# Kernel tuning notes

Measured on AMD Instinct MI355X. Metric: run time of the kernel, lower is better.

## Reference

```python
import jax, jax.numpy as jnp
import numpy as np

N_HEADS = 16
N_KV_HEADS = 4
HEAD_DIM = 128  # n_embd // n_head = 2048 // 16
NEG_INF = -1e9


def setup_inputs() -> dict:
    key = jax.random.key(0)
    ks = jax.random.split(key, 4)
    B, T, C = 8, 1024, 2048
    x = jax.random.normal(ks[0], (B, T, C), dtype=jnp.float32)
    sc = 1.0 / np.sqrt(C)
    Wq = jax.random.normal(ks[1], (C, C), dtype=jnp.float32) * sc
    bq = jnp.zeros((C,), dtype=jnp.float32)
    Wkv = jax.random.normal(ks[2], (N_KV_HEADS * HEAD_DIM * 2, C), dtype=jnp.float32) * sc
    bkv = jnp.zeros((N_KV_HEADS * HEAD_DIM * 2,), dtype=jnp.float32)
    Wo = jax.random.normal(ks[3], (C, C), dtype=jnp.float32) * sc
    bo = jnp.zeros((C,), dtype=jnp.float32)
    return {"x": x, "Wq": Wq, "bq": bq, "Wkv": Wkv, "bkv": bkv, "Wo": Wo, "bo": bo}


def reference(x, Wq, bq, Wkv, bkv, Wo, bo):
    B, T, C = x.shape
    g = N_HEADS // N_KV_HEADS  # group size for repeat_interleave
    # q: [B, H, T, D]
    q = (x @ Wq.T + bq).reshape(B, T, N_HEADS, HEAD_DIM).transpose(0, 2, 1, 3)
    # kv: [B, T, Hkv, 2, D] -> [B, Hkv, T, 2, D]
    kv = (x @ Wkv.T + bkv).reshape(B, T, N_KV_HEADS, 2, HEAD_DIM).transpose(0, 2, 1, 3, 4)
    k = kv[..., 0, :]  # [B, Hkv, T, D]
    v = kv[..., 1, :]
    # repeat_interleave along head dim to expand kv heads to full heads
    k = jnp.repeat(k, g, axis=1)  # [B, H, T, D]
    v = jnp.repeat(v, g, axis=1)
    scale = 1.0 / jnp.sqrt(jnp.asarray(HEAD_DIM, dtype=x.dtype))
    scores = jnp.einsum('bhqd,bhkd->bhqk', q, k) * scale  # [B, H, T, T]
    causal = jnp.tril(jnp.ones((T, T), dtype=bool))
    scores = jnp.where(causal[None, None], scores, NEG_INF)
    attn = jax.nn.softmax(scores, axis=-1)
    y = jnp.einsum('bhqk,bhkd->bhqd', attn, v)  # [B, H, T, D]
    y = y.transpose(0, 2, 1, 3).reshape(B, T, C)
    return y @ Wo.T + bo
```

## Files before the change

kernel.cpp:

```cpp
#include <hip/hip_runtime.h>

typedef short short8 __attribute__((ext_vector_type(8)));
typedef short short4v __attribute__((ext_vector_type(4)));
typedef float floatx4 __attribute__((ext_vector_type(4)));
typedef unsigned short ushort_t;
typedef unsigned int uint_t;

#define DI __device__ __forceinline__

DI ushort_t f2bf(float f) {
  uint_t u = __builtin_bit_cast(uint_t, f);
  uint_t r = u + 0x7FFFu + ((u >> 16) & 1u);
  return (ushort_t)(r >> 16);
}

DI float exp2a(float x) {
  float r;
  asm("v_exp_f32 %0, %1" : "=v"(r) : "v"(x));
  return r;
}

DI floatx4 mfma16(short8 a, short8 b, floatx4 c) {
  return __builtin_amdgcn_mfma_f32_16x16x32_bf16(a, b, c, 0, 0, 0);
}

DI void async16(const void* g, void* l) {
  __builtin_amdgcn_global_load_lds(
      (__attribute__((address_space(1))) void*)(g),
      (__attribute__((address_space(3))) void*)(l), 16, 0, 0);
}

DI void cfence() { asm volatile("" ::: "memory"); }

__global__ __launch_bounds__(256)
void k_f2bf(const float* __restrict__ in, ushort_t* __restrict__ out, long n)
{
  const long i = ((long)blockIdx.x * 256 + threadIdx.x) * 8;
  if (i >= n) return;
  const float4 a = *(const float4*)(in + i);
  const float4 b = *(const float4*)(in + i + 4);
  union { short8 s; ushort_t u[8]; } o;
  o.u[0] = f2bf(a.x); o.u[1] = f2bf(a.y); o.u[2] = f2bf(a.z); o.u[3] = f2bf(a.w);
  o.u[4] = f2bf(b.x); o.u[5] = f2bf(b.y); o.u[6] = f2bf(b.z); o.u[7] = f2bf(b.w);
  *(short8*)(out + i) = o.s;
}

template<int OUT_BF16>
__global__ __launch_bounds__(256)
void k_gemm(const ushort_t* __restrict__ A, const ushort_t* __restrict__ B,
            const float* __restrict__ bias, void* __restrict__ Cout,
            int N, int K, float out_scale)
{
  __shared__ __align__(16) ushort_t As[4][128 * 32];
  __shared__ __align__(16) ushort_t Bs[4][128 * 32];
  const int tid = threadIdx.x;
  const int w = tid >> 6, l = tid & 63;
  const int wm = w >> 1, wn = w & 1;
  const int lr = l & 15, lg = l >> 4;
  const long m0 = (long)blockIdx.y * 128;
  const long n0 = (long)blockIdx.x * 128;

  const floatx4 fz = {0.f, 0.f, 0.f, 0.f};
  floatx4 acc[4][4];
#pragma unroll
  for (int i = 0; i < 4; ++i)
#pragma unroll
    for (int j = 0; j < 4; ++j) acc[i][j] = fz;

  const int c0 = tid, c1 = 256 + tid;
  const int r0 = c0 >> 2, r1 = c1 >> 2;
  const ushort_t* gA0 = A + (m0 + r0) * K + (((c0 & 3) ^ (r0 & 3)) << 3);
  const ushort_t* gA1 = A + (m0 + r1) * K + (((c1 & 3) ^ (r1 & 3)) << 3);
  const ushort_t* gB0 = B + (n0 + r0) * K + (((c0 & 3) ^ (r0 & 3)) << 3);
  const ushort_t* gB1 = B + (n0 + r1) * K + (((c1 & 3) ^ (r1 & 3)) << 3);

  const int nK = K >> 5;
#pragma unroll
  for (int pt = 0; pt < 3; ++pt) {
    const int ko = pt << 5;
    async16(gA0 + ko, &As[pt][c0 * 8]);
    async16(gA1 + ko, &As[pt][c1 * 8]);
    async16(gB0 + ko, &Bs[pt][c0 * 8]);
    async16(gB1 + ko, &Bs[pt][c1 * 8]);
  }

  const int xg = (lr & 3);

  for (int kt = 0; kt < nK; ++kt) {
    const int cur = kt & 3;
    const int rem = nK - 1 - kt;
    if (rem >= 3) {
      const int ko = (kt + 3) << 5;
      const int nb = (kt + 3) & 3;
      async16(gA0 + ko, &As[nb][c0 * 8]);
      async16(gA1 + ko, &As[nb][c1 * 8]);
      async16(gB0 + ko, &Bs[nb][c0 * 8]);
      async16(gB1 + ko, &Bs[nb][c1 * 8]);
      asm volatile("s_waitcnt vmcnt(12)" ::: "memory");
    } else if (rem == 2) {
      asm volatile("s_waitcnt vmcnt(8)" ::: "memory");
    } else if (rem == 1) {
      asm volatile("s_waitcnt vmcnt(4)" ::: "memory");
    } else {
      asm volatile("s_waitcnt vmcnt(0)" ::: "memory");
    }
    __builtin_amdgcn_s_barrier();
    cfence();

    short8 a[4], b[4];
#pragma unroll
    for (int i = 0; i < 4; ++i)
      a[i] = *(const short8*)&As[cur][(wm * 64 + i * 16 + lr) * 32 + ((lg ^ xg) * 8)];
#pragma unroll
    for (int j = 0; j < 4; ++j)
      b[j] = *(const short8*)&Bs[cur][(wn * 64 + j * 16 + lr) * 32 + ((lg ^ xg) * 8)];
#pragma unroll
    for (int i = 0; i < 4; ++i)
#pragma unroll
      for (int j = 0; j < 4; ++j)
        acc[i][j] = mfma16(a[i], b[j], acc[i][j]);

    asm volatile("s_waitcnt lgkmcnt(0)" ::: "memory");
    __builtin_amdgcn_s_barrier();
    cfence();
  }

#pragma unroll
  for (int j = 0; j < 4; ++j) {
    const long gn = n0 + wn * 64 + j * 16 + lr;
    const float bv = bias[gn];
#pragma unroll
    for (int i = 0; i < 4; ++i) {
      const long gm = m0 + wm * 64 + i * 16 + lg * 4;
#pragma unroll
      for (int r = 0; r < 4; ++r) {
        const float v = (acc[i][j][r] + bv) * out_scale;
        if (OUT_BF16) ((ushort_t*)Cout)[(gm + r) * N + gn] = f2bf(v);
        else          ((float*)Cout)[(gm + r) * N + gn] = v;
      }
    }
  }
}

#define STG_A2(t_, h_, bf_) do { \
    async16(aS + (h_)*128*K + (t_)*64,        &Al[bf_][(h_)*8192 + dD]); \
    async16(aS + ((h_)*128+64)*K + (t_)*64,   &Al[bf_][(h_)*8192 + 4096 + dD]); } while(0)
#define STG_B2(t_, h_, bf_) do { \
    async16(bS + (h_)*128*K + (t_)*64,        &Bl[bf_][(h_)*8192 + dD]); \
    async16(bS + ((h_)*128+64)*K + (t_)*64,   &Bl[bf_][(h_)*8192 + 4096 + dD]); } while(0)
#define LDA2(bf_, mh_) { _Pragma("unroll") for (int i = 0; i < 4; ++i) { \
    aA[i] = *(const short8*)&Al[bf_][raB + ((mh_)*4+i)*1024 + g0]; \
    aB[i] = *(const short8*)&Al[bf_][raB + ((mh_)*4+i)*1024 + g1]; } }
#define LDB2_0(bf_) { _Pragma("unroll") for (int j = 0; j < 2; ++j) { \
    bA0[j] = *(const short8*)&Bl[bf_][rbB + j*1024 + g0]; \
    bB0[j] = *(const short8*)&Bl[bf_][rbB + j*1024 + g1]; } }
#define LDB2_1(bf_) { _Pragma("unroll") for (int j = 0; j < 2; ++j) { \
    bA1[j] = *(const short8*)&Bl[bf_][rbB + (2+j)*1024 + g0]; \
    bB1[j] = *(const short8*)&Bl[bf_][rbB + (2+j)*1024 + g1]; } }
#define MFQ2(mh_, nh_, bA_, bB_) { _Pragma("unroll") for (int i = 0; i < 4; ++i) \
    _Pragma("unroll") for (int j = 0; j < 2; ++j) { \
      acc[(mh_)*4+i][(nh_)*2+j] = mfma16(aA[i], bA_[j], acc[(mh_)*4+i][(nh_)*2+j]); \
      acc[(mh_)*4+i][(nh_)*2+j] = mfma16(aB[i], bB_[j], acc[(mh_)*4+i][(nh_)*2+j]); } }
#define WAITV2(n_) asm volatile("s_waitcnt vmcnt(" #n_ ")" ::: "memory")
#define BARC      { __builtin_amdgcn_s_barrier(); cfence(); }
#define PRIO1     __builtin_amdgcn_s_setprio(1)
#define PRIO0     __builtin_amdgcn_s_setprio(0)

template<int OUT_BF16>
__global__ __launch_bounds__(512, 2)
void k_gemm2(const ushort_t* __restrict__ A, const ushort_t* __restrict__ B,
             const float* __restrict__ bias, void* __restrict__ Cout,
             int N, int K, int gx, float out_scale)
{
  __shared__ __align__(16) ushort_t Al[2][256 * 64];
  __shared__ __align__(16) ushort_t Bl[2][256 * 64];
  const int tid = threadIdx.x;
  const int w = tid >> 6, l = tid & 63;
  const int wr = w >> 2, wc = w & 3;
  const int lr = l & 15, lg = l >> 4;

  const int nwg = gridDim.x;
  const int qd = nwg >> 3;
  const int p = blockIdx.x;
  const int swz = (p & 7) * qd + (p >> 3);
  const long m0 = (long)(swz / gx) * 256;
  const long n0 = (long)(swz % gx) * 256;

  const floatx4 fz = {0.f, 0.f, 0.f, 0.f};
  floatx4 acc[8][4];
#pragma unroll
  for (int i = 0; i < 8; ++i)
#pragma unroll
    for (int j = 0; j < 4; ++j) acc[i][j] = fz;

  const int rowL = tid >> 3, s = tid & 7;
  const int sx = s ^ (rowL & 7);
  const ushort_t* aS = A + (m0 + rowL) * K + sx * 8;
  const ushort_t* bS = B + (n0 + rowL) * K + sx * 8;
  const int dD = rowL * 64 + s * 8;

  const int raB = (wr * 128 + lr) * 64;
  const int rbB = (wc * 64 + lr) * 64;
  const int x8 = lr & 7;
  const int g0 = (lg ^ x8) * 8;
  const int g1 = ((4 + lg) ^ x8) * 8;

  short8 aA[4], aB[4], bA0[2], bB0[2], bA1[2], bB1[2];

  const int nT = K >> 6;
  STG_A2(0, 0, 0);
  STG_B2(0, 0, 0);
  STG_B2(0, 1, 0);
  STG_A2(0, 1, 0);
  WAITV2(4); BARC;

  for (int t = 0; t < nT - 1; ++t) {
    const int cur = t & 1, nxt = cur ^ 1;
    LDA2(cur, 0); LDB2_0(cur);
    STG_A2(t + 1, 0, nxt);
    BARC;
    PRIO1; MFQ2(0, 0, bA0, bB0); PRIO0;
    WAITV2(4); BARC;
    LDB2_1(cur);
    STG_B2(t + 1, 0, nxt);
    BARC;
    PRIO1; MFQ2(0, 1, bA1, bB1); PRIO0;
    WAITV2(4); BARC;
    LDA2(cur, 1);
    STG_B2(t + 1, 1, nxt);
    BARC;
    PRIO1; MFQ2(1, 1, bA1, bB1); PRIO0;
    BARC;
    STG_A2(t + 1, 1, nxt);
    PRIO1; MFQ2(1, 0, bA0, bB0); PRIO0;
    WAITV2(4); BARC;
  }
  {
    const int cur = (nT - 1) & 1;
    LDA2(cur, 0); LDB2_0(cur);
    PRIO1; MFQ2(0, 0, bA0, bB0); PRIO0;
    WAITV2(2); BARC;
    LDB2_1(cur);
    PRIO1; MFQ2(0, 1, bA1, bB1); PRIO0;
    WAITV2(0); BARC;
    LDA2(cur, 1);
    PRIO1; MFQ2(1, 1, bA1, bB1); MFQ2(1, 0, bA0, bB0); PRIO0;
  }

#pragma unroll
  for (int j = 0; j < 4; ++j) {
    const long gn = n0 + wc * 64 + j * 16 + lr;
    const float bv = bias[gn];
#pragma unroll
    for (int i = 0; i < 8; ++i) {
      const long gm = m0 + wr * 128 + i * 16 + lg * 4;
#pragma unroll
      for (int r = 0; r < 4; ++r) {
        const float v = (acc[i][j][r] + bv) * out_scale;
        if (OUT_BF16) ((ushort_t*)Cout)[(gm + r) * N + gn] = f2bf(v);
        else          ((float*)Cout)[(gm + r) * N + gn] = v;
      }
    }
  }
}

__global__ __launch_bounds__(256)
void k_transv(const ushort_t* __restrict__ KV, ushort_t* __restrict__ Vt)
{
  const int tblk = blockIdx.x, kh = blockIdx.y, b = blockIdx.z;
  const int tid = threadIdx.x;
#pragma unroll
  for (int j = 0; j < 4; ++j) {
    const int c = j * 256 + tid;
    const int d = c >> 3, t0 = (c & 7) << 3;
    const ushort_t* src = KV + (long)(b * 1024 + tblk * 64 + t0) * 1024 + kh * 256 + 128 + d;
    union { short8 s; ushort_t u[8]; } vv;
#pragma unroll
    for (int i = 0; i < 8; ++i) vv.u[i] = src[(long)i * 1024];
    *(short8*)(Vt + ((long)(b * 4 + kh) * 128 + d) * 1024 + tblk * 64 + t0) = vv.s;
  }
}

__global__ __launch_bounds__(256)
void k_attn(const ushort_t* __restrict__ Q, const ushort_t* __restrict__ KV,
            const ushort_t* __restrict__ Vt, ushort_t* __restrict__ Y)
{
  __shared__ __align__(16) ushort_t Kl[2][64 * 128];
  __shared__ __align__(16) ushort_t Vl[2][128 * 64];
  __shared__ __align__(16) ushort_t Pl[4][16][72];
  const int tid = threadIdx.x;
  const int w = tid >> 6, l = tid & 63;
  const int lr = l & 15, lg = l >> 4;
  const int p = blockIdx.x;
  const int v = ((p & 7) << 8) | (p >> 3);
  const int b = v >> 8;
  const int kh = (v >> 6) & 3;
  const int hs = (v >> 4) & 3;
  const int qt = 15 - (v & 15);
  const int h = kh * 4 + hs;
  const int qrow = qt * 64 + w * 16;

  const ushort_t* qptr = Q + ((long)(b * 1024 + qrow + lr)) * 2048 + h * 128 + lg * 8;
  short8 qf[4];
#pragma unroll
  for (int c = 0; c < 4; ++c) qf[c] = *(const short8*)(qptr + c * 32);

  const ushort_t* kg[4];
  const ushort_t* vg[4];
  int ld[4];
#pragma unroll
  for (int i = 0; i < 4; ++i) {
    const int c = i * 256 + tid;
    const int row = c >> 4, sgk = (c & 15) ^ (row & 7);
    kg[i] = KV + ((long)(b * 1024 + row)) * 1024 + kh * 256 + sgk * 8;
    const int d = c >> 3, sgv = (c & 7) ^ (d & 7);
    vg[i] = Vt + ((long)((b * 4 + kh) * 128 + d)) * 1024 + sgv * 8;
    ld[i] = c * 8;
  }

  float m_s = 0.f;
  float l_p = 0.f;
  const floatx4 fz = {0.f, 0.f, 0.f, 0.f};
  floatx4 yacc[8];
#pragma unroll
  for (int dt = 0; dt < 8; ++dt) yacc[dt] = fz;

  const int xk = (lr & 7) << 4;

#pragma unroll
  for (int i = 0; i < 4; ++i) async16(kg[i], &Kl[0][ld[i]]);
#pragma unroll
  for (int i = 0; i < 4; ++i) async16(vg[i], &Vl[0][ld[i]]);

  for (int t = 0; t <= qt; ++t) {
    const ushort_t* KlC = &Kl[t & 1][0];
    const ushort_t* VlC = &Vl[t & 1][0];
    asm volatile("s_waitcnt vmcnt(0)" ::: "memory");
    asm volatile("s_waitcnt lgkmcnt(0)" ::: "memory");
    __builtin_amdgcn_s_barrier();
    cfence();
    if (t < qt) {
      const long ko = (long)(t + 1) * 65536;
      const long vo = (long)(t + 1) * 64;
      ushort_t* KlN = &Kl[(t + 1) & 1][0];
      ushort_t* VlN = &Vl[(t + 1) & 1][0];
#pragma unroll
      for (int i = 0; i < 4; ++i) async16(kg[i] + ko, &KlN[ld[i]]);
#pragma unroll
      for (int i = 0; i < 4; ++i) async16(vg[i] + vo, &VlN[ld[i]]);
    }

    const floatx4 finit = {-m_s, -m_s, -m_s, -m_s};
    floatx4 st[4];
#pragma unroll
    for (int k2 = 0; k2 < 4; ++k2) {
      floatx4 sacc = finit;
      const int row = k2 * 16 + lr;
#pragma unroll
      for (int c = 0; c < 4; ++c) {
        const int off = row * 256 + ((c * 64 + lg * 16) ^ xk);
        const short8 kf = *(const short8*)((const char*)KlC + off);
        sacc = mfma16(kf, qf[c], sacc);
      }
      st[k2] = sacc;
    }
    if (t == qt) {
      const int qg = qrow + lr;
#pragma unroll
      for (int k2 = 0; k2 < 4; ++k2)
#pragma unroll
        for (int r = 0; r < 4; ++r)
          if (t * 64 + k2 * 16 + lg * 4 + r > qg) st[k2][r] = -__builtin_inff();
    }
    float pm = -__builtin_inff();
#pragma unroll
    for (int k2 = 0; k2 < 4; ++k2)
      pm = fmaxf(pm, fmaxf(fmaxf(st[k2][0], st[k2][1]), fmaxf(st[k2][2], st[k2][3])));
    if (!__all(pm <= 8.f)) {
      float pmf = fmaxf(pm, __shfl_xor(pm, 16));
      pmf = fmaxf(pmf, __shfl_xor(pmf, 32));
      const float d = fmaxf(pmf, 0.f);
      m_s += d;
      const float corr = exp2a(-d);
      l_p *= corr;
      const float cc0 = __shfl(corr, lg * 4 + 0);
      const float cc1 = __shfl(corr, lg * 4 + 1);
      const float cc2 = __shfl(corr, lg * 4 + 2);
      const float cc3 = __shfl(corr, lg * 4 + 3);
#pragma unroll
      for (int dt = 0; dt < 8; ++dt) {
        yacc[dt][0] *= cc0; yacc[dt][1] *= cc1;
        yacc[dt][2] *= cc2; yacc[dt][3] *= cc3;
      }
#pragma unroll
      for (int k2 = 0; k2 < 4; ++k2)
#pragma unroll
        for (int r = 0; r < 4; ++r) st[k2][r] -= d;
    }
    float psum = 0.f;
#pragma unroll
    for (int k2 = 0; k2 < 4; ++k2) {
      const float pe0 = exp2a(st[k2][0]);
      const float pe1 = exp2a(st[k2][1]);
      const float pe2 = exp2a(st[k2][2]);
      const float pe3 = exp2a(st[k2][3]);
      psum += (pe0 + pe1) + (pe2 + pe3);
      uint_t d0, d1;
      asm("v_cvt_pk_bf16_f32 %0, %1, %2" : "=v"(d0) : "v"(pe0), "v"(pe1));
      asm("v_cvt_pk_bf16_f32 %0, %1, %2" : "=v"(d1) : "v"(pe2), "v"(pe3));
      uint2 pkv; pkv.x = d0; pkv.y = d1;
      *(uint2*)&Pl[w][lr][k2 * 16 + lg * 4] = pkv;
    }
    l_p += psum;
    asm volatile("s_waitcnt lgkmcnt(0)" ::: "memory");

#pragma unroll
    for (int kc = 0; kc < 2; ++kc) {
      const short8 pf = *(const short8*)&Pl[w][lr][kc * 32 + lg * 8];
#pragma unroll
      for (int dt = 0; dt < 8; ++dt) {
        const int d = dt * 16 + lr;
        const int off = d * 128 + ((kc * 64 + lg * 16) ^ xk);
        const short8 vf = *(const short8*)((const char*)VlC + off);
        yacc[dt] = mfma16(pf, vf, yacc[dt]);
      }
    }
    cfence();
  }

  float l_s = l_p;
  l_s += __shfl_xor(l_s, 16);
  l_s += __shfl_xor(l_s, 32);
  const float linv = 1.f / l_s;
  const float i0 = __shfl(linv, lg * 4 + 0);
  const float i1 = __shfl(linv, lg * 4 + 1);
  const float i2 = __shfl(linv, lg * 4 + 2);
  const float i3 = __shfl(linv, lg * 4 + 3);
  ushort_t* yp = Y + ((long)(b * 1024 + qrow)) * 2048 + h * 128 + lr;
#pragma unroll
  for (int dt = 0; dt < 8; ++dt) {
    yp[(long)(lg * 4 + 0) * 2048 + dt * 16] = f2bf(yacc[dt][0] * i0);
    yp[(long)(lg * 4 + 1) * 2048 + dt * 16] = f2bf(yacc[dt][1] * i1);
    yp[(long)(lg * 4 + 2) * 2048 + dt * 16] = f2bf(yacc[dt][2] * i2);
    yp[(long)(lg * 4 + 3) * 2048 + dt * 16] = f2bf(yacc[dt][3] * i3);
  }
}

extern "C" void kernel_launch(void* const* d_in, const int* in_sizes, int n_in,
                              void* d_out, int out_size, void* d_ws, size_t ws_size,
                              hipStream_t stream)
{
  (void)in_sizes; (void)n_in; (void)out_size;
  const float* x   = (const float*)d_in[0];
  const float* Wq  = (const float*)d_in[1];
  const float* bq  = (const float*)d_in[2];
  const float* Wkv = (const float*)d_in[3];
  const float* bkv = (const float*)d_in[4];
  const float* Wo  = (const float*)d_in[5];
  const float* bo  = (const float*)d_in[6];
  float* out = (float*)d_out;
  char* ws = (char*)d_ws;

  if (ws_size < 104857600) return;

  const long NX = 8192L * 2048, NWQ = 2048L * 2048, NWKV = 1024L * 2048, NWO = 2048L * 2048;
  ushort_t* xb   = (ushort_t*)(ws);
  ushort_t* Qb   = (ushort_t*)(ws + 33554432);
  ushort_t* KVb  = (ushort_t*)(ws + 67108864);
  ushort_t* Wqb  = (ushort_t*)(ws + 83886080);
  ushort_t* Wkvb = (ushort_t*)(ws + 92274688);
  ushort_t* Wob  = (ushort_t*)(ws + 96468992);
  ushort_t* Vtb  = Wqb;
  ushort_t* Yb   = xb;

  k_f2bf<<<dim3(NX   / 2048), 256, 0, stream>>>(x,   xb,   NX);
  k_f2bf<<<dim3(NWQ  / 2048), 256, 0, stream>>>(Wq,  Wqb,  NWQ);
  k_f2bf<<<dim3(NWKV / 2048), 256, 0, stream>>>(Wkv, Wkvb, NWKV);
  k_f2bf<<<dim3(NWO  / 2048), 256, 0, stream>>>(Wo,  Wob,  NWO);

  const float scale = 0.12751743f;
  k_gemm2<1><<<dim3(256), 512, 0, stream>>>(xb, Wqb,  bq,  Qb,  2048, 2048, 8, scale);
  k_gemm<1><<<dim3(8, 64), 256, 0, stream>>>(xb, Wkvb, bkv, KVb, 1024, 2048, 1.0f);
  k_transv<<<dim3(16, 4, 8), 256, 0, stream>>>(KVb, Vtb);
  k_attn<<<dim3(2048), 256, 0, stream>>>(Qb, KVb, Vtb, Yb);
  k_gemm2<0><<<dim3(256), 512, 0, stream>>>(Yb, Wob, bo, out, 2048, 2048, 8, 1.0f);
}
```

Before: 314.8 us.

## Simplify GEMM main loop to a single barrier per K-tile

```diff
diff --git a/kernel.cpp b/kernel.cpp
--- a/kernel.cpp
+++ b/kernel.cpp
@@ -161,8 +161,6 @@
     _Pragma("unroll") for (int j = 0; j < 2; ++j) { \
       acc[(mh_)*4+i][(nh_)*2+j] = mfma16(aA[i], bA_[j], acc[(mh_)*4+i][(nh_)*2+j]); \
       acc[(mh_)*4+i][(nh_)*2+j] = mfma16(aB[i], bB_[j], acc[(mh_)*4+i][(nh_)*2+j]); } }
-#define WAITV2(n_) asm volatile("s_waitcnt vmcnt(" #n_ ")" ::: "memory")
-#define BARC      { __builtin_amdgcn_s_barrier(); cfence(); }
 #define PRIO1     __builtin_amdgcn_s_setprio(1)
 #define PRIO0     __builtin_amdgcn_s_setprio(0)
 
@@ -212,39 +210,25 @@
   STG_B2(0, 0, 0);
   STG_B2(0, 1, 0);
   STG_A2(0, 1, 0);
-  WAITV2(4); BARC;
-
-  for (int t = 0; t < nT - 1; ++t) {
+  asm volatile("s_waitcnt vmcnt(0)" ::: "memory");
+  __builtin_amdgcn_s_barrier();
+  cfence();
+
+  for (int t = 0; t < nT; ++t) {
     const int cur = t & 1, nxt = cur ^ 1;
-    LDA2(cur, 0); LDB2_0(cur);
-    STG_A2(t + 1, 0, nxt);
-    BARC;
-    PRIO1; MFQ2(0, 0, bA0, bB0); PRIO0;
-    WAITV2(4); BARC;
-    LDB2_1(cur);
-    STG_B2(t + 1, 0, nxt);
-    BARC;
-    PRIO1; MFQ2(0, 1, bA1, bB1); PRIO0;
-    WAITV2(4); BARC;
-    LDA2(cur, 1);
-    STG_B2(t + 1, 1, nxt);
-    BARC;
-    PRIO1; MFQ2(1, 1, bA1, bB1); PRIO0;
-    BARC;
-    STG_A2(t + 1, 1, nxt);
-    PRIO1; MFQ2(1, 0, bA0, bB0); PRIO0;
-    WAITV2(4); BARC;
-  }
-  {
-    const int cur = (nT - 1) & 1;
+    const bool pre = (t + 1 < nT);
+    if (pre) { STG_A2(t + 1, 0, nxt); STG_B2(t + 1, 0, nxt); }
     LDA2(cur, 0); LDB2_0(cur);
     PRIO1; MFQ2(0, 0, bA0, bB0); PRIO0;
-    WAITV2(2); BARC;
+    if (pre) { STG_B2(t + 1, 1, nxt); STG_A2(t + 1, 1, nxt); }
     LDB2_1(cur);
     PRIO1; MFQ2(0, 1, bA1, bB1); PRIO0;
-    WAITV2(0); BARC;
     LDA2(cur, 1);
-    PRIO1; MFQ2(1, 1, bA1, bB1); MFQ2(1, 0, bA0, bB0); PRIO0;
+    PRIO1; MFQ2(1, 1, bA1, bB1); PRIO0;
+    PRIO1; MFQ2(1, 0, bA0, bB0); PRIO0;
+    asm volatile("s_waitcnt vmcnt(0)" ::: "memory");
+    __builtin_amdgcn_s_barrier();
+    cfence();
   }
 
 #pragma unroll
```

New measurement: 318.5 us. Within noise of the previous version (+1.2%).
